# Kernel tuning notes

Measured on AMD Instinct MI355X. Metric: run time of the kernel, lower is better.

## Reference

```python
import jax, jax.numpy as jnp
from jax import lax
import numpy as np


def setup_inputs() -> dict:
    key = jax.random.key(0)
    N, T = 2_000_000, 32
    probs = jax.random.uniform(key, (N, T), dtype=jnp.float32)
    return {"probs": probs}


def reference(probs):
    # Faithful to the torch loop:
    #   s_{-1} = 0;  s_i = (s_{i-1} + p_i) * prod_{j != i} (1 - p_j)
    #   loss = -sum_n s_{t-1} / n
    one_minus = 1.0 - probs  # [n, t]
    # leave-one-out products Q_i = prod_{j != i} (1 - p_j) via exclusive prefix/suffix cumprods
    prefix = jnp.cumprod(one_minus, axis=1)
    excl_prefix = jnp.concatenate(
        [jnp.ones_like(prefix[:, :1]), prefix[:, :-1]], axis=1)
    suffix = jnp.cumprod(one_minus[:, ::-1], axis=1)[:, ::-1]
    excl_suffix = jnp.concatenate(
        [suffix[:, 1:], jnp.ones_like(suffix[:, :1])], axis=1)
    q = excl_prefix * excl_suffix  # [n, t]

    def step(s, pq):
        p_i, q_i = pq  # each [n]
        return (s + p_i) * q_i, None

    s0 = jnp.zeros(probs.shape[0], dtype=probs.dtype)
    s, _ = lax.scan(step, s0, (probs.T, q.T))  # scan over t classes
    return -jnp.sum(s) / probs.shape[0]
```

## Files before the change

### kernel.cpp

```cpp
#include <hip/hip_runtime.h>

#define T 32
#define BLOCK 256
#define GRID 2048

__global__ __launch_bounds__(BLOCK) void mel_rows(const float* __restrict__ probs,
                                                  double* __restrict__ partials,
                                                  int nrows) {
    const int tid = blockIdx.x * blockDim.x + threadIdx.x;
    const int stride = gridDim.x * blockDim.x;

    double acc = 0.0;
    for (int row = tid; row < nrows; row += stride) {
        const float4* rp = reinterpret_cast<const float4*>(probs + (size_t)row * T);
        float p[T];
        #pragma unroll
        for (int k = 0; k < T / 4; ++k) {
            float4 v = rp[k];
            p[4 * k + 0] = v.x;
            p[4 * k + 1] = v.y;
            p[4 * k + 2] = v.z;
            p[4 * k + 3] = v.w;
        }

        float suf[T];
        suf[T - 1] = 1.0f;
        #pragma unroll
        for (int i = T - 2; i >= 0; --i) suf[i] = suf[i + 1] * (1.0f - p[i + 1]);

        float pre = 1.0f;
        float s = 0.0f;
        #pragma unroll
        for (int i = 0; i < T; ++i) {
            float q = pre * suf[i];
            s = (s + p[i]) * q;
            pre *= (1.0f - p[i]);
        }
        acc += (double)s;
    }

    #pragma unroll
    for (int off = 32; off > 0; off >>= 1)
        acc += __shfl_down(acc, off, 64);

    __shared__ double sdata[BLOCK / 64];
    const int lane = threadIdx.x & 63;
    const int wid = threadIdx.x >> 6;
    if (lane == 0) sdata[wid] = acc;
    __syncthreads();
    if (threadIdx.x == 0) {
        double b = 0.0;
        #pragma unroll
        for (int w = 0; w < BLOCK / 64; ++w) b += sdata[w];
        partials[blockIdx.x] = b;
    }
}

__global__ __launch_bounds__(BLOCK) void mel_final(const double* __restrict__ partials,
                                                   float* __restrict__ out,
                                                   int nrows) {
    double acc = 0.0;
    for (int i = threadIdx.x; i < GRID; i += BLOCK) acc += partials[i];

    #pragma unroll
    for (int off = 32; off > 0; off >>= 1)
        acc += __shfl_down(acc, off, 64);

    __shared__ double sdata[BLOCK / 64];
    const int lane = threadIdx.x & 63;
    const int wid = threadIdx.x >> 6;
    if (lane == 0) sdata[wid] = acc;
    __syncthreads();
    if (threadIdx.x == 0) {
        double b = 0.0;
        #pragma unroll
        for (int w = 0; w < BLOCK / 64; ++w) b += sdata[w];
        out[0] = (float)(-b / (double)nrows);
    }
}

extern "C" void kernel_launch(void* const* d_in, const int* in_sizes, int n_in,
                              void* d_out, int out_size, void* d_ws, size_t ws_size,
                              hipStream_t stream) {
    const float* probs = (const float*)d_in[0];
    float* out = (float*)d_out;
    double* partials = (double*)d_ws;
    const int nrows = in_sizes[0] / T;

    mel_rows<<<GRID, BLOCK, 0, stream>>>(probs, partials, nrows);
    mel_final<<<1, BLOCK, 0, stream>>>(partials, out, nrows);
}
```

Before: 45.04 us.

## Stage rows through LDS with direct global-to-LDS loads and fuse final reduction

Each block now loads a 256-row chunk into a swizzled LDS tile using global_load_lds, so the global reads are fully coalesced instead of each thread reading its own 128-byte row. Threads then read their row from LDS with an XOR swizzle to avoid bank conflicts. The separate final-reduction kernel is replaced by a fixed-point 64-bit atomic accumulation and a last-block-done counter, which removes one launch but adds a memset and atomics. The fixed-point scaling could lose precision or overflow for unusual inputs.

```diff
diff --git a/kernel.cpp b/kernel.cpp
--- a/kernel.cpp
+++ b/kernel.cpp
@@ -4,23 +4,50 @@
 #define BLOCK 256
 #define GRID 2048
 
-__global__ __launch_bounds__(BLOCK) void mel_rows(const float* __restrict__ probs,
-                                                  double* __restrict__ partials,
-                                                  int nrows) {
-    const int tid = blockIdx.x * blockDim.x + threadIdx.x;
-    const int stride = gridDim.x * blockDim.x;
+typedef float v4f __attribute__((ext_vector_type(4)));
+
+__global__ __launch_bounds__(BLOCK) void mel_fused(const float* __restrict__ probs,
+                                                   int nrows, int nlaunched,
+                                                   unsigned long long* __restrict__ ws,
+                                                   float* __restrict__ out) {
+    __shared__ float lds[BLOCK * T];
+    __shared__ double sred[BLOCK / 64];
+
+    const int t = threadIdx.x;
+    const int w = t >> 6;
+    const int l = t & 63;
+    const int nchunks = (nrows + BLOCK - 1) / BLOCK;
+    const long long maxf4 = (long long)nrows * (T / 4) - 1;
+
+    const int lrow8 = l >> 3;
+    const int lseg  = (l & 7) ^ lrow8;
+    const int sw    = t & 7;
+    const int rbase = t * T;
 
     double acc = 0.0;
-    for (int row = tid; row < nrows; row += stride) {
-        const float4* rp = reinterpret_cast<const float4*>(probs + (size_t)row * T);
+
+    for (int c = blockIdx.x; c < nchunks; c += gridDim.x) {
+        const long long chunkF4 = (long long)c * BLOCK * (T / 4);
+
+        #pragma unroll
+        for (int k = 0; k < 8; ++k) {
+            long long srcF4 = chunkF4 + (long long)((w * 64 + k * 8 + lrow8) * 8 + lseg);
+            if (srcF4 > maxf4) srcF4 = maxf4;
+            __builtin_amdgcn_global_load_lds(
+                (const __attribute__((address_space(1))) void*)((const v4f*)probs + srcF4),
+                (__attribute__((address_space(3))) void*)&lds[(w * 8 + k) * 256],
+                16, 0, 0);
+        }
+        asm volatile("s_waitcnt vmcnt(0)" ::: "memory");
+
         float p[T];
         #pragma unroll
-        for (int k = 0; k < T / 4; ++k) {
-            float4 v = rp[k];
-            p[4 * k + 0] = v.x;
-            p[4 * k + 1] = v.y;
-            p[4 * k + 2] = v.z;
-            p[4 * k + 3] = v.w;
+        for (int i = 0; i < T / 4; ++i) {
+            v4f v = *(const v4f*)&lds[rbase + 4 * (i ^ sw)];
+            p[4 * i + 0] = v[0];
+            p[4 * i + 1] = v[1];
+            p[4 * i + 2] = v[2];
+            p[4 * i + 3] = v[3];
         }
 
         float suf[T];
@@ -28,54 +55,33 @@
         #pragma unroll
         for (int i = T - 2; i >= 0; --i) suf[i] = suf[i + 1] * (1.0f - p[i + 1]);
 
-        float pre = 1.0f;
-        float s = 0.0f;
+        float pre = 1.0f, s = 0.0f;
         #pragma unroll
         for (int i = 0; i < T; ++i) {
             float q = pre * suf[i];
             s = (s + p[i]) * q;
             pre *= (1.0f - p[i]);
         }
-        acc += (double)s;
+
+        if ((long long)c * BLOCK + t < nrows) acc += (double)s;
     }
 
     #pragma unroll
-    for (int off = 32; off > 0; off >>= 1)
-        acc += __shfl_down(acc, off, 64);
-
-    __shared__ double sdata[BLOCK / 64];
-    const int lane = threadIdx.x & 63;
-    const int wid = threadIdx.x >> 6;
-    if (lane == 0) sdata[wid] = acc;
+    for (int off = 32; off > 0; off >>= 1) acc += __shfl_down(acc, off, 64);
+    if (l == 0) sred[w] = acc;
     __syncthreads();
-    if (threadIdx.x == 0) {
-        double b = 0.0;
-        #pragma unroll
-        for (int w = 0; w < BLOCK / 64; ++w) b += sdata[w];
-        partials[blockIdx.x] = b;
-    }
-}
-
-__global__ __launch_bounds__(BLOCK) void mel_final(const double* __restrict__ partials,
-                                                   float* __restrict__ out,
-                                                   int nrows) {
-    double acc = 0.0;
-    for (int i = threadIdx.x; i < GRID; i += BLOCK) acc += partials[i];
-
-    #pragma unroll
-    for (int off = 32; off > 0; off >>= 1)
-        acc += __shfl_down(acc, off, 64);
-
-    __shared__ double sdata[BLOCK / 64];
-    const int lane = threadIdx.x & 63;
-    const int wid = threadIdx.x >> 6;
-    if (lane == 0) sdata[wid] = acc;
-    __syncthreads();
-    if (threadIdx.x == 0) {
-        double b = 0.0;
-        #pragma unroll
-        for (int w = 0; w < BLOCK / 64; ++w) b += sdata[w];
-        out[0] = (float)(-b / (double)nrows);
+    if (t == 0) {
+        double b = sred[0] + sred[1] + sred[2] + sred[3];
+        long long fx = __double2ll_rn(b * 68719476736.0);
+        atomicAdd(ws, (unsigned long long)fx);
+        __threadfence();
+        unsigned int old = atomicAdd((unsigned int*)(ws + 1), 1u);
+        if (old == (unsigned int)(nlaunched - 1)) {
+            __threadfence();
+            unsigned long long tot = atomicAdd(ws, 0ULL);
+            double total = (double)(long long)tot * (1.0 / 68719476736.0);
+            out[0] = (float)(-total / (double)nrows);
+        }
     }
 }
 
@@ -84,9 +90,11 @@
                               hipStream_t stream) {
     const float* probs = (const float*)d_in[0];
     float* out = (float*)d_out;
-    double* partials = (double*)d_ws;
     const int nrows = in_sizes[0] / T;
+    const int nchunks = (nrows + BLOCK - 1) / BLOCK;
+    const int grid = (GRID < nchunks) ? GRID : nchunks;
 
-    mel_rows<<<GRID, BLOCK, 0, stream>>>(probs, partials, nrows);
-    mel_final<<<1, BLOCK, 0, stream>>>(partials, out, nrows);
+    hipMemsetAsync(d_ws, 0, 16, stream);
+    mel_fused<<<grid, BLOCK, 0, stream>>>(probs, nrows, grid,
+                                          (unsigned long long*)d_ws, out);
 }
```

Result: slower. 106.5 us (+136.4%).
